# Optimization experiments

Measured on AMD Instinct MI355X. Metric: run time of the kernel, lower is better.

## Reference

```python
import jax, jax.numpy as jnp
import numpy as np

N = 4096      # 2 ** var_num, var_num = 12
L = 50        # trajectory length
A_NUM = 4     # number of action variables (len(id2actvar))


def setup_inputs() -> dict:
    key = jax.random.key(0)
    ks = jax.random.split(key, 6)
    scale = 0.5 / np.sqrt(N)  # keep recurrence spectrally stable over L steps
    return {
        "init_states": jax.random.normal(ks[0], (N,), dtype=jnp.float32),
        "trajectories": jax.random.uniform(ks[1], (L, A_NUM), dtype=jnp.float32),
        "T_base": jax.random.normal(ks[2], (N, N), dtype=jnp.float32) * scale,
        "A_mats": jax.random.normal(ks[3], (A_NUM, N, N), dtype=jnp.float32) * (scale / A_NUM),
        "b": jax.random.normal(ks[4], (N,), dtype=jnp.float32) * 0.1,
        "r": jax.random.normal(ks[5], (N,), dtype=jnp.float32),
    }


def reference(init_states, trajectories, T_base, A_mats, b, r):
    # init_states is read from x in the original model but never used in the loop.
    n = T_base.shape[0]
    interface0 = jnp.zeros((n,), dtype=T_base.dtype)  # tf.zeros(2**var_num)

    def step(old_interface, act):
        # action-conditioned circuit filter: T_t = T_base + sum_a act[a] * A_mats[a]
        T = T_base + jnp.einsum('a,anm->nm', act, A_mats)
        new_interface = T @ old_interface + b          # [N]
        exp_reward = jnp.sum(r * new_interface)        # tf.reduce_sum(exp_reward)
        return new_interface, exp_reward

    _, exp_rewards = jax.lax.scan(step, interface0, trajectories)
    return exp_rewards  # [L]
```

## Files before the change

### kernel.cpp

```cpp
#include <hip/hip_runtime.h>
#include <hip/hip_fp16.h>

#define NDIM   4096
#define LSTEPS 50
#define ANUM   4
#define NN     ((size_t)NDIM * (size_t)NDIM)
#define ROWQ   512
#define RSTRIDE (5 * ROWQ)
#define LDSQ   128

#define NBLOCKS 1024
#define GRPS    16
#define BPG     (NBLOCKS / GRPS)

typedef unsigned int nuint4 __attribute__((ext_vector_type(4)));

#define MAT_BYTES ((size_t)(5 * NN * sizeof(__half)))
#define X_BYTES   ((size_t)(LSTEPS + 1) * NDIM * sizeof(float))
#define BAR_LINES 33
#define BAR_BYTES ((size_t)BAR_LINES * 128)

__device__ __forceinline__ void grid_barrier(unsigned* __restrict__ bar, int bid) {
    __syncthreads();
    if (threadIdx.x == 0) {
        const int grp = bid & (GRPS - 1);
        unsigned* genp = bar + (size_t)(17 + grp) * 32;
        const unsigned g = __hip_atomic_load(genp, __ATOMIC_RELAXED,
                                             __HIP_MEMORY_SCOPE_AGENT);
        const unsigned prev = __hip_atomic_fetch_add(bar + (size_t)(1 + grp) * 32, 1u,
                                   __ATOMIC_RELAXED, __HIP_MEMORY_SCOPE_AGENT);
        if ((prev & (BPG - 1)) == (unsigned)(BPG - 1)) {
            const unsigned rp = __hip_atomic_fetch_add(bar, 1u,
                                   __ATOMIC_RELAXED, __HIP_MEMORY_SCOPE_AGENT);
            if ((rp & (GRPS - 1)) == (unsigned)(GRPS - 1)) {
#pragma unroll
                for (int i = 0; i < GRPS; i++)
                    __hip_atomic_fetch_add(bar + (size_t)(17 + i) * 32, 1u,
                        __ATOMIC_RELAXED, __HIP_MEMORY_SCOPE_AGENT);
            }
        }
        int spins = 0;
        while (__hip_atomic_load(genp, __ATOMIC_RELAXED,
                                 __HIP_MEMORY_SCOPE_AGENT) == g) {
            __builtin_amdgcn_s_sleep(2);
            if (++spins > (1 << 20)) break;
        }
    }
    __syncthreads();
}

__global__ void init_bar_kernel(unsigned* __restrict__ bar) {
    for (int i = threadIdx.x; i < BAR_LINES * 32; i += 256) bar[i] = 0u;
}

__device__ __forceinline__ void fma5(const nuint4 v[5], const float4 xa,
                                     const float4 xb, float acc[5]) {
#pragma unroll
    for (int m = 0; m < 5; m++) {
        union { nuint4 v; __half2 h2[4]; } u;
        u.v = v[m];
        const float2 p0 = __half22float2(u.h2[0]);
        const float2 p1 = __half22float2(u.h2[1]);
        const float2 p2 = __half22float2(u.h2[2]);
        const float2 p3 = __half22float2(u.h2[3]);
        float a = acc[m];
        a = fmaf(p0.x, xa.x, a); a = fmaf(p0.y, xa.y, a);
        a = fmaf(p1.x, xa.z, a); a = fmaf(p1.y, xa.w, a);
        a = fmaf(p2.x, xb.x, a); a = fmaf(p2.y, xb.y, a);
        a = fmaf(p3.x, xb.z, a); a = fmaf(p3.y, xb.w, a);
        acc[m] = a;
    }
}

__global__ __launch_bounds__(256, 4) void fused_kernel(
        const float* __restrict__ Tb, const float* __restrict__ Am,
        const float* __restrict__ b,  const float* __restrict__ r,
        const float* __restrict__ traj,
        uint4* __restrict__ mats, float* __restrict__ xs,
        unsigned* __restrict__ bar, float* __restrict__ out) {
    const int tid = threadIdx.x;
    const int bid = blockIdx.x;

    __shared__ nuint4 cache[4][5][LDSQ];

    {
        const size_t dstBase = (size_t)bid * (4 * RSTRIDE);
#pragma unroll 4
        for (int k = 0; k < 40; k++) {
            const int off = tid + 256 * k;
            const int rowLocal = off / RSTRIDE;
            const int rem = off - rowLocal * RSTRIDE;
            const int m = rem >> 9;
            const int c = rem & 511;
            const int row = bid * 4 + rowLocal;
            const float* src = (m == 0) ? Tb : (Am + (size_t)(m - 1) * NN);
            const float4* s4 = (const float4*)src;
            const size_t fi = (size_t)row * 1024 + 2 * (size_t)c;
            const float4 f0 = s4[fi];
            const float4 f1 = s4[fi + 1];
            union { nuint4 v; __half h[8]; } pk;
            pk.h[0] = __float2half(f0.x); pk.h[1] = __float2half(f0.y);
            pk.h[2] = __float2half(f0.z); pk.h[3] = __float2half(f0.w);
            pk.h[4] = __float2half(f1.x); pk.h[5] = __float2half(f1.y);
            pk.h[6] = __float2half(f1.z); pk.h[7] = __float2half(f1.w);
            __builtin_nontemporal_store(pk.v, (nuint4*)&mats[dstBase + off]);
            if (c < LDSQ) cache[rowLocal][m][c] = pk.v;
        }
        if (tid < 4)
            __hip_atomic_store(&xs[NDIM + bid * 4 + tid], b[bid * 4 + tid],
                               __ATOMIC_RELAXED, __HIP_MEMORY_SCOPE_AGENT);
    }
    grid_barrier(bar, bid);
    __threadfence();

    const int wave = tid >> 6, lane = tid & 63;
    const int row  = bid * 4 + wave;
    const size_t base = (size_t)row * RSTRIDE;
    const nuint4* M = (const nuint4*)mats;
    const float4* trajv = (const float4*)traj;

    for (int t = 1; t < LSTEPS; t++) {
        const float4* xv = (const float4*)(xs + (size_t)t * NDIM);
        const float4 av = trajv[t];
        float acc[5] = {0.f, 0.f, 0.f, 0.f, 0.f};

#pragma unroll
        for (int c = 0; c < 2; c++) {
            const int ci = c * 64 + lane;
            const float4 xa = xv[ci * 2];
            const float4 xb = xv[ci * 2 + 1];
            nuint4 v[5];
#pragma unroll
            for (int m = 0; m < 5; m++) v[m] = cache[wave][m][ci];
            fma5(v, xa, xb, acc);
        }
        if (t & 1) {
#pragma unroll
            for (int cc = 0; cc < 6; cc++) {
                const int ci = (2 + cc) * 64 + lane;
                const float4 xa = xv[ci * 2];
                const float4 xb = xv[ci * 2 + 1];
                nuint4 v[5];
#pragma unroll
                for (int m = 0; m < 5; m++) v[m] = M[base + (size_t)m * ROWQ + ci];
                fma5(v, xa, xb, acc);
            }
        } else {
#pragma unroll
            for (int cc = 5; cc >= 0; cc--) {
                const int ci = (2 + cc) * 64 + lane;
                const float4 xa = xv[ci * 2];
                const float4 xb = xv[ci * 2 + 1];
                nuint4 v[5];
#pragma unroll
                for (int m = 0; m < 5; m++) v[m] = M[base + (size_t)m * ROWQ + ci];
                fma5(v, xa, xb, acc);
            }
        }

        float s = acc[0] + av.x * acc[1] + av.y * acc[2] + av.z * acc[3] + av.w * acc[4];
#pragma unroll
        for (int o = 32; o > 0; o >>= 1) s += __shfl_xor(s, o, 64);
        if (lane == 0)
            __hip_atomic_store(&xs[(size_t)(t + 1) * NDIM + row], s + b[row],
                               __ATOMIC_RELAXED, __HIP_MEMORY_SCOPE_AGENT);
        grid_barrier(bar, bid);
    }

    if (bid < LSTEPS) {
        float* parts = (float*)cache;
        const float* x = xs + (size_t)(bid + 1) * NDIM;
        float s = 0.f;
#pragma unroll
        for (int i = 0; i < 16; i++) {
            const int idx = tid + 256 * i;
            s = fmaf(r[idx], x[idx], s);
        }
#pragma unroll
        for (int o = 32; o > 0; o >>= 1) s += __shfl_xor(s, o, 64);
        if (lane == 0) parts[wave] = s;
        __syncthreads();
        if (tid == 0) out[bid] = parts[0] + parts[1] + parts[2] + parts[3];
    }
}

__global__ void init_kernel(const float* __restrict__ b, float* __restrict__ x1) {
    const int tid = threadIdx.x;
    const float4* bv = (const float4*)b;
    float4* xv = (float4*)x1;
#pragma unroll
    for (int i = 0; i < 4; i++) xv[tid + 256 * i] = bv[tid + 256 * i];
}

__global__ void dot_kernel(const float* __restrict__ x, const float* __restrict__ r,
                           float* __restrict__ out_elem) {
    const int tid = threadIdx.x;
    const int wave = tid >> 6, lane = tid & 63;
    __shared__ float parts[4];
    float s = 0.f;
#pragma unroll
    for (int i = 0; i < 16; i++) {
        const int idx = tid + 256 * i;
        s = fmaf(r[idx], x[idx], s);
    }
#pragma unroll
    for (int off = 32; off > 0; off >>= 1) s += __shfl_xor(s, off, 64);
    if (lane == 0) parts[wave] = s;
    __syncthreads();
    if (tid == 0) *out_elem = parts[0] + parts[1] + parts[2] + parts[3];
}

__global__ __launch_bounds__(256) void step_f32_kernel(
        const float* __restrict__ Tb, const float* __restrict__ Am,
        const float* __restrict__ x_in, float* __restrict__ x_out,
        const float* __restrict__ b, const float* __restrict__ r,
        const float* __restrict__ traj, float* __restrict__ out, int t) {
    const int tid  = threadIdx.x;
    const int wave = tid >> 6, lane = tid & 63;
    __shared__ float parts[4];

    if (blockIdx.x == gridDim.x - 1) {
        float s = 0.f;
#pragma unroll
        for (int i = 0; i < 16; i++) {
            const int idx = tid + 256 * i;
            s = fmaf(r[idx], x_in[idx], s);
        }
#pragma unroll
        for (int off = 32; off > 0; off >>= 1) s += __shfl_xor(s, off, 64);
        if (lane == 0) parts[wave] = s;
        __syncthreads();
        if (tid == 0) out[t - 1] = parts[0] + parts[1] + parts[2] + parts[3];
        return;
    }

    const float a0 = traj[t * ANUM + 0], a1 = traj[t * ANUM + 1],
                a2 = traj[t * ANUM + 2], a3 = traj[t * ANUM + 3];
    const int row = blockIdx.x * 4 + wave;
    const float4* mat[5] = {
        (const float4*)Tb, (const float4*)Am, (const float4*)(Am + NN),
        (const float4*)(Am + 2 * NN), (const float4*)(Am + 3 * NN)};
    const size_t rowq = (size_t)row * (NDIM / 4);
    const float4* xv = (const float4*)x_in;

    float acc[5] = {0.f, 0.f, 0.f, 0.f, 0.f};
#pragma unroll
    for (int c = 0; c < 16; c++) {
        const int ci = c * 64 + lane;
        const float4 xa = xv[ci];
        const size_t qi = rowq + ci;
#pragma unroll
        for (int m = 0; m < 5; m++) {
            const float4 v = mat[m][qi];
            float a = acc[m];
            a = fmaf(v.x, xa.x, a); a = fmaf(v.y, xa.y, a);
            a = fmaf(v.z, xa.z, a); a = fmaf(v.w, xa.w, a);
            acc[m] = a;
        }
    }
    float s = acc[0] + a0 * acc[1] + a1 * acc[2] + a2 * acc[3] + a3 * acc[4];
#pragma unroll
    for (int off = 32; off > 0; off >>= 1) s += __shfl_xor(s, off, 64);
    if (lane == 0) x_out[row] = s + b[row];
}

extern "C" void kernel_launch(void* const* d_in, const int* in_sizes, int n_in,
                              void* d_out, int out_size, void* d_ws, size_t ws_size,
                              hipStream_t stream) {
    const float* traj = (const float*)d_in[1];
    const float* Tb   = (const float*)d_in[2];
    const float* Am   = (const float*)d_in[3];
    const float* b    = (const float*)d_in[4];
    const float* r    = (const float*)d_in[5];
    float* out = (float*)d_out;

    const size_t need = MAT_BYTES + X_BYTES + BAR_BYTES;

    if (ws_size >= need) {
        uint4*    mats = (uint4*)d_ws;
        float*    xs   = (float*)((char*)d_ws + MAT_BYTES);
        unsigned* bar  = (unsigned*)((char*)d_ws + MAT_BYTES + X_BYTES);
        init_bar_kernel<<<1, 256, 0, stream>>>(bar);
        fused_kernel<<<NBLOCKS, 256, 0, stream>>>(Tb, Am, b, r, traj,
                                                  mats, xs, bar, out);
    } else {
        float* x0 = (float*)d_ws;
        float* x1 = x0 + NDIM;
        init_kernel<<<1, 256, 0, stream>>>(b, x0);
        for (int t = 1; t < LSTEPS; t++) {
            float* xi = (t & 1) ? x0 : x1;
            float* xo = (t & 1) ? x1 : x0;
            step_f32_kernel<<<NDIM / 4 + 1, 256, 0, stream>>>(Tb, Am, xi, xo, b, r,
                                                              traj, out, t);
        }
        dot_kernel<<<1, 256, 0, stream>>>(x1, r, out + (LSTEPS - 1));
    }
}
```

Baseline: 1.611 ms.

## Split each row across two waves in 512-thread cooperative persistent kernel

Adds a 512-thread-per-block persistent kernel in which two waves share each row, each covering half the columns. The two partial sums are combined through a small global scratch buffer before the grid barrier. It is launched cooperatively so co-residency is guaranteed, with the old 256-thread kernel kept as a fallback. It also replaces the nontemporal stores of the half-precision matrix copy with normal stores and lowers the barrier spin limit. The aim is more waves in flight to hide the memory latency of the per-step matrix-vector product, at the cost of an extra cross-wave reduction and a cooperative-launch requirement for 1024 blocks of 512 threads.

New measurement: 1.864 ms. +15.7%, slower.

```diff
diff --git a/kernel.cpp b/kernel.cpp
--- a/kernel.cpp
+++ b/kernel.cpp
@@ -12,6 +12,7 @@
 #define NBLOCKS 1024
 #define GRPS    16
 #define BPG     (NBLOCKS / GRPS)
+#define SPIN_MAX (1 << 17)
 
 typedef unsigned int nuint4 __attribute__((ext_vector_type(4)));
 
@@ -19,6 +20,7 @@
 #define X_BYTES   ((size_t)(LSTEPS + 1) * NDIM * sizeof(float))
 #define BAR_LINES 33
 #define BAR_BYTES ((size_t)BAR_LINES * 128)
+#define XPART_BYTES ((size_t)NBLOCKS * 8 * sizeof(float))
 
 __device__ __forceinline__ void grid_barrier(unsigned* __restrict__ bar, int bid) {
     __syncthreads();
@@ -43,7 +45,7 @@
         while (__hip_atomic_load(genp, __ATOMIC_RELAXED,
                                  __HIP_MEMORY_SCOPE_AGENT) == g) {
             __builtin_amdgcn_s_sleep(2);
-            if (++spins > (1 << 20)) break;
+            if (++spins > SPIN_MAX) break;
         }
     }
     __syncthreads();
@@ -72,7 +74,160 @@
     }
 }
 
-__global__ __launch_bounds__(256, 4) void fused_kernel(
+__global__ __launch_bounds__(512, 8) void fused512_kernel(
+        const float* __restrict__ Tb, const float* __restrict__ Am,
+        const float* __restrict__ b,  const float* __restrict__ r,
+        const float* __restrict__ traj,
+        uint4* __restrict__ mats, float* __restrict__ xs,
+        unsigned* __restrict__ bar, float* __restrict__ xpart,
+        float* __restrict__ out) {
+    const int tid = threadIdx.x;
+    const int bid = blockIdx.x;
+
+    __shared__ nuint4 cache[4][5][2][64];
+
+    {
+        const size_t dstBase = (size_t)bid * (4 * RSTRIDE);
+#pragma unroll 4
+        for (int k = 0; k < 20; k++) {
+            const int off = tid + 512 * k;
+            const int rowLocal = off / RSTRIDE;
+            const int rem = off - rowLocal * RSTRIDE;
+            const int m = rem >> 9;
+            const int c = rem & 511;
+            const int row = bid * 4 + rowLocal;
+            const float* src = (m == 0) ? Tb : (Am + (size_t)(m - 1) * NN);
+            const float4* s4 = (const float4*)src;
+            const size_t fi = (size_t)row * 1024 + 2 * (size_t)c;
+            const float4 f0 = s4[fi];
+            const float4 f1 = s4[fi + 1];
+            union { nuint4 v; __half h[8]; } pk;
+            pk.h[0] = __float2half(f0.x); pk.h[1] = __float2half(f0.y);
+            pk.h[2] = __float2half(f0.z); pk.h[3] = __float2half(f0.w);
+            pk.h[4] = __float2half(f1.x); pk.h[5] = __float2half(f1.y);
+            pk.h[6] = __float2half(f1.z); pk.h[7] = __float2half(f1.w);
+            ((nuint4*)mats)[dstBase + off] = pk.v;
+            const int grp = c >> 6;
+            if (grp == 0) cache[rowLocal][m][0][c & 63] = pk.v;
+            if (grp == 4) cache[rowLocal][m][1][c & 63] = pk.v;
+        }
+        if (tid < 4)
+            __hip_atomic_store(&xs[NDIM + bid * 4 + tid], b[bid * 4 + tid],
+                               __ATOMIC_RELAXED, __HIP_MEMORY_SCOPE_AGENT);
+    }
+    grid_barrier(bar, bid);
+    __threadfence();
+
+    const int w = tid >> 6, lane = tid & 63;
+    const int rowLocal = w >> 1, half = w & 1;
+    const int row  = bid * 4 + rowLocal;
+    const size_t base = (size_t)row * RSTRIDE;
+    const int glds = half * 4;
+    const nuint4* M = (const nuint4*)mats;
+    const float4* trajv = (const float4*)traj;
+
+    for (int t = 1; t < LSTEPS; t++) {
+        const float4* xv = (const float4*)(xs + (size_t)t * NDIM);
+        const float4 av = trajv[t];
+        float acc[5] = {0.f, 0.f, 0.f, 0.f, 0.f};
+
+        {
+            const int ci = glds * 64 + lane;
+            nuint4 v[5];
+#pragma unroll
+            for (int m = 0; m < 5; m++) v[m] = cache[rowLocal][m][half][lane];
+            fma5(v, xv[ci * 2], xv[ci * 2 + 1], acc);
+        }
+        if (t & 1) {
+#pragma unroll
+            for (int cc = 0; cc < 3; cc++) {
+                const int ci = (glds + 1 + cc) * 64 + lane;
+                nuint4 v[5];
+#pragma unroll
+                for (int m = 0; m < 5; m++) v[m] = M[base + (size_t)m * ROWQ + ci];
+                fma5(v, xv[ci * 2], xv[ci * 2 + 1], acc);
+            }
+        } else {
+#pragma unroll
+            for (int cc = 2; cc >= 0; cc--) {
+                const int ci = (glds + 1 + cc) * 64 + lane;
+                nuint4 v[5];
+#pragma unroll
+                for (int m = 0; m < 5; m++) v[m] = M[base + (size_t)m * ROWQ + ci];
+                fma5(v, xv[ci * 2], xv[ci * 2 + 1], acc);
+            }
+        }
+
+        float s = acc[0] + av.x * acc[1] + av.y * acc[2] + av.z * acc[3] + av.w * acc[4];
+#pragma unroll
+        for (int o = 32; o > 0; o >>= 1) s += __shfl_xor(s, o, 64);
+        if (lane == 0)
+            __hip_atomic_store(&xpart[bid * 8 + w], s,
+                               __ATOMIC_RELAXED, __HIP_MEMORY_SCOPE_AGENT);
+        __syncthreads();
+        if (tid < 4) {
+            const int rr = bid * 4 + tid;
+            const float p0 = __hip_atomic_load(&xpart[bid * 8 + 2 * tid],
+                                __ATOMIC_RELAXED, __HIP_MEMORY_SCOPE_AGENT);
+            const float p1 = __hip_atomic_load(&xpart[bid * 8 + 2 * tid + 1],
+                                __ATOMIC_RELAXED, __HIP_MEMORY_SCOPE_AGENT);
+            __hip_atomic_store(&xs[(size_t)(t + 1) * NDIM + rr], p0 + p1 + b[rr],
+                               __ATOMIC_RELAXED, __HIP_MEMORY_SCOPE_AGENT);
+        }
+        grid_barrier(bar, bid);
+    }
+
+    if (bid < LSTEPS) {
+        float* parts = (float*)cache;
+        const float* x = xs + (size_t)(bid + 1) * NDIM;
+        float s = 0.f;
+#pragma unroll
+        for (int i = 0; i < 8; i++) {
+            const int idx = tid + 512 * i;
+            s = fmaf(r[idx], x[idx], s);
+        }
+#pragma unroll
+        for (int o = 32; o > 0; o >>= 1) s += __shfl_xor(s, o, 64);
+        if (lane == 0) parts[w] = s;
+        __syncthreads();
+        if (tid == 0) {
+            float tot = 0.f;
+#pragma unroll
+            for (int i = 0; i < 8; i++) tot += parts[i];
+            out[bid] = tot;
+        }
+    }
+}
+
+template<bool ASC>
+__device__ __forceinline__ float step_row256(const nuint4* __restrict__ M,
+        const size_t base, const nuint4 (* __restrict__ cacheRow)[LDSQ],
+        const float4* __restrict__ xv, const int lane, const float4 av) {
+    float acc[5] = {0.f, 0.f, 0.f, 0.f, 0.f};
+#pragma unroll
+    for (int c = 0; c < 2; c++) {
+        const int ci = c * 64 + lane;
+        nuint4 v[5];
+#pragma unroll
+        for (int m = 0; m < 5; m++) v[m] = cacheRow[m][ci];
+        fma5(v, xv[ci * 2], xv[ci * 2 + 1], acc);
+    }
+#pragma unroll
+    for (int cc = 0; cc < 6; cc++) {
+        const int g  = ASC ? (2 + cc) : (7 - cc);
+        const int ci = g * 64 + lane;
+        nuint4 v[5];
+#pragma unroll
+        for (int m = 0; m < 5; m++) v[m] = M[base + (size_t)m * ROWQ + ci];
+        fma5(v, xv[ci * 2], xv[ci * 2 + 1], acc);
+    }
+    float s = acc[0] + av.x * acc[1] + av.y * acc[2] + av.z * acc[3] + av.w * acc[4];
+#pragma unroll
+    for (int o = 32; o > 0; o >>= 1) s += __shfl_xor(s, o, 64);
+    return s;
+}
+
+__global__ __launch_bounds__(256, 4) void fused256_kernel(
         const float* __restrict__ Tb, const float* __restrict__ Am,
         const float* __restrict__ b,  const float* __restrict__ r,
         const float* __restrict__ traj,
@@ -103,7 +258,7 @@
             pk.h[2] = __float2half(f0.z); pk.h[3] = __float2half(f0.w);
             pk.h[4] = __float2half(f1.x); pk.h[5] = __float2half(f1.y);
             pk.h[6] = __float2half(f1.z); pk.h[7] = __float2half(f1.w);
-            __builtin_nontemporal_store(pk.v, (nuint4*)&mats[dstBase + off]);
+            ((nuint4*)mats)[dstBase + off] = pk.v;
             if (c < LDSQ) cache[rowLocal][m][c] = pk.v;
         }
         if (tid < 4)
@@ -122,45 +277,9 @@
     for (int t = 1; t < LSTEPS; t++) {
         const float4* xv = (const float4*)(xs + (size_t)t * NDIM);
         const float4 av = trajv[t];
-        float acc[5] = {0.f, 0.f, 0.f, 0.f, 0.f};
-
-#pragma unroll
-        for (int c = 0; c < 2; c++) {
-            const int ci = c * 64 + lane;
-            const float4 xa = xv[ci * 2];
-            const float4 xb = xv[ci * 2 + 1];
-            nuint4 v[5];
-#pragma unroll
-            for (int m = 0; m < 5; m++) v[m] = cache[wave][m][ci];
-            fma5(v, xa, xb, acc);
-        }
-        if (t & 1) {
-#pragma unroll
-            for (int cc = 0; cc < 6; cc++) {
-                const int ci = (2 + cc) * 64 + lane;
-                const float4 xa = xv[ci * 2];
-                const float4 xb = xv[ci * 2 + 1];
-                nuint4 v[5];
-#pragma unroll
-                for (int m = 0; m < 5; m++) v[m] = M[base + (size_t)m * ROWQ + ci];
-                fma5(v, xa, xb, acc);
-            }
-        } else {
-#pragma unroll
-            for (int cc = 5; cc >= 0; cc--) {
-                const int ci = (2 + cc) * 64 + lane;
-                const float4 xa = xv[ci * 2];
-                const float4 xb = xv[ci * 2 + 1];
-                nuint4 v[5];
-#pragma unroll
-                for (int m = 0; m < 5; m++) v[m] = M[base + (size_t)m * ROWQ + ci];
-                fma5(v, xa, xb, acc);
-            }
-        }
-
-        float s = acc[0] + av.x * acc[1] + av.y * acc[2] + av.z * acc[3] + av.w * acc[4];
-#pragma unroll
-        for (int o = 32; o > 0; o >>= 1) s += __shfl_xor(s, o, 64);
+        const float s = (t & 1)
+            ? step_row256<true >(M, base, cache[wave], xv, lane, av)
+            : step_row256<false>(M, base, cache[wave], xv, lane, av);
         if (lane == 0)
             __hip_atomic_store(&xs[(size_t)(t + 1) * NDIM + row], s + b[row],
                                __ATOMIC_RELAXED, __HIP_MEMORY_SCOPE_AGENT);
@@ -274,15 +393,26 @@
     const float* r    = (const float*)d_in[5];
     float* out = (float*)d_out;
 
-    const size_t need = MAT_BYTES + X_BYTES + BAR_BYTES;
+    const size_t need = MAT_BYTES + X_BYTES + BAR_BYTES + XPART_BYTES;
 
     if (ws_size >= need) {
-        uint4*    mats = (uint4*)d_ws;
-        float*    xs   = (float*)((char*)d_ws + MAT_BYTES);
-        unsigned* bar  = (unsigned*)((char*)d_ws + MAT_BYTES + X_BYTES);
+        uint4*    mats  = (uint4*)d_ws;
+        float*    xs    = (float*)((char*)d_ws + MAT_BYTES);
+        unsigned* bar   = (unsigned*)((char*)d_ws + MAT_BYTES + X_BYTES);
+        float*    xpart = (float*)((char*)d_ws + MAT_BYTES + X_BYTES + BAR_BYTES);
         init_bar_kernel<<<1, 256, 0, stream>>>(bar);
-        fused_kernel<<<NBLOCKS, 256, 0, stream>>>(Tb, Am, b, r, traj,
-                                                  mats, xs, bar, out);
+
+        void* args[] = {(void*)&Tb, (void*)&Am, (void*)&b, (void*)&r,
+                        (void*)&traj, (void*)&mats, (void*)&xs, (void*)&bar,
+                        (void*)&xpart, (void*)&out};
+        hipError_t ce = hipLaunchCooperativeKernel(
+            (const void*)fused512_kernel, dim3(NBLOCKS), dim3(512),
+            args, 0, stream);
+        if (ce != hipSuccess) {
+            (void)hipGetLastError();
+            fused256_kernel<<<NBLOCKS, 256, 0, stream>>>(Tb, Am, b, r, traj,
+                                                         mats, xs, bar, out);
+        }
     } else {
         float* x0 = (float*)d_ws;
         float* x1 = x0 + NDIM;
```
